# Performance work log

Hardware: AMD Instinct MI355X
Metric: run time of the kernel (lower is better)

## Reference

```python
import jax, jax.numpy as jnp
import numpy as np

N_NODES = 100000


def _gcn_norm(edge_index, n):
    # PyG GCNConv default: add self-loops, symmetric normalization
    src, dst = edge_index[0], edge_index[1]
    loops = jnp.arange(n, dtype=src.dtype)
    src = jnp.concatenate([src, loops])
    dst = jnp.concatenate([dst, loops])
    deg = jax.ops.segment_sum(jnp.ones_like(dst, dtype=jnp.float32), dst, num_segments=n)
    dinv = jnp.where(deg > 0, jax.lax.rsqrt(deg), 0.0)
    norm = dinv[src] * dinv[dst]  # [E+N]
    return src, dst, norm


def _gcn_conv(x, src, dst, norm, W, b, n):
    h = x @ W                                  # [N, out] transform first
    msg = h[src] * norm[:, None]               # gather + edge weight
    out = jax.ops.segment_sum(msg, dst, num_segments=n)  # scatter-add
    return out + b


def setup_inputs() -> dict:
    key = jax.random.key(0)
    k1, k2, k3, k4 = jax.random.split(key, 4)
    in_f, h_f, out_f = 128, 256, 128
    x = jax.random.normal(k1, (N_NODES, in_f), dtype=jnp.float32)
    edge_index = jax.random.randint(k2, (2, 1600000), 0, N_NODES, dtype=jnp.int64)
    W1 = jax.random.normal(k3, (in_f, h_f), dtype=jnp.float32) / np.sqrt(in_f)
    b1 = jnp.zeros((h_f,), dtype=jnp.float32)
    W2 = jax.random.normal(k4, (h_f, out_f), dtype=jnp.float32) / np.sqrt(h_f)
    b2 = jnp.zeros((out_f,), dtype=jnp.float32)
    return {"x": x, "edge_index": edge_index, "W1": W1, "b1": b1, "W2": W2, "b2": b2}


def reference(x, edge_index, W1, b1, W2, b2):
    n = x.shape[0]
    src, dst, norm = _gcn_norm(edge_index, n)
    h = jax.nn.relu(_gcn_conv(x, src, dst, norm, W1, b1, n))
    return _gcn_conv(h, src, dst, norm, W2, b2, n)
```

## Files before the change

kernel.cpp:

```cpp
#include <hip/hip_runtime.h>

typedef __bf16 bf16x8 __attribute__((ext_vector_type(8)));
typedef float f32x4 __attribute__((ext_vector_type(4)));

#define DEVI static __device__ __forceinline__
#define CHUNK 4096
#define SCH 8192

DEVI unsigned short f2bf(float f){
  unsigned int x = __builtin_bit_cast(unsigned int, f);
  x = (x + 0x7fffu + ((x >> 16) & 1u)) >> 16;
  return (unsigned short)x;
}
DEVI unsigned int packbf2(float a, float b){
  return (unsigned int)f2bf(a) | ((unsigned int)f2bf(b) << 16);
}
DEVI float bflo(unsigned int u){ return __builtin_bit_cast(float, u << 16); }
DEVI float bfhi(unsigned int u){ return __builtin_bit_cast(float, u & 0xffff0000u); }

__global__ void k_zero(int* __restrict__ p, int n){
  int i = blockIdx.x*256 + threadIdx.x;
  if (i < n) p[i] = 0;
}


__global__ __launch_bounds__(256) void kb_hist(const int* __restrict__ dst,
    int* __restrict__ bucketCnt, int E, int NB){
  __shared__ int h[2048];
  for (int i=threadIdx.x;i<NB;i+=256) h[i]=0;
  __syncthreads();
  int base = blockIdx.x*CHUNK;
  int lim = base+CHUNK < E ? base+CHUNK : E;
  for (int i = base+threadIdx.x; i < lim; i += 256)
    atomicAdd(&h[dst[i]>>8], 1);
  __syncthreads();
  for (int i=threadIdx.x;i<NB;i+=256)
    if (h[i]) atomicAdd(&bucketCnt[i], h[i]);
}

__global__ __launch_bounds__(256) void kb_scan(const int* __restrict__ bucketCnt,
    int* __restrict__ bucketOff, int* __restrict__ bucketCur,
    int* __restrict__ cCur, int NB, int NBC){
  __shared__ int sh[256];
  int t = threadIdx.x;
  int per = (NB+255)/256;
  int vals[8];
  int lsum = 0;
  for (int j=0;j<per;j++){
    int i = t*per+j;
    int v = (i<NB) ? bucketCnt[i] : 0;
    vals[j]=v; lsum+=v;
  }
  sh[t]=lsum; __syncthreads();
  for (int off=1; off<256; off<<=1){
    int x = (t>=off) ? sh[t-off] : 0;
    __syncthreads();
    sh[t] += x;
    __syncthreads();
  }
  int run = sh[t]-lsum;
  for (int j=0;j<per;j++){
    int i = t*per+j;
    if (i<NB){ bucketOff[i]=run; bucketCur[i]=run; }
    run += vals[j];
  }
  if (t==255) bucketOff[NB]=run;
  __syncthreads();
  for (int c=t;c<NBC;c+=256){
    int f = c*8;
    cCur[c] = bucketOff[f < NB ? f : NB];
  }
}

__global__ __launch_bounds__(512) void kb_scat1(const int* __restrict__ src,
    const int* __restrict__ dst, int* __restrict__ cur,
    int* __restrict__ p1, int E, int NBK){
  __shared__ int h[64];
  __shared__ int baseSh[64];
  int t = threadIdx.x;
  if (t < NBK){ h[t]=0; }
  __syncthreads();
  int base = blockIdx.x*SCH;
  int lim = base+SCH < E ? base+SCH : E;
  for (int i = base+t; i < lim; i += 512)
    atomicAdd(&h[dst[i]>>11], 1);
  __syncthreads();
  if (t < NBK){
    int c = h[t];
    baseSh[t] = c ? atomicAdd(&cur[t], c) : 0;
    h[t] = 0;
  }
  __syncthreads();
  for (int i = base+t; i < lim; i += 512){
    int d = dst[i];
    int b = d>>11;
    int r = atomicAdd(&h[b], 1);
    int p = baseSh[b] + r;
    p1[p] = (src[i]<<11) | (d & 2047);
  }
}

__global__ __launch_bounds__(512) void kb_scat2(const int* __restrict__ p1,
    const int* __restrict__ bOff, int* __restrict__ cur,
    int* __restrict__ pk, int NB){
  __shared__ int h[8];
  __shared__ int baseSh[8];
  int t = threadIdx.x;
  int bc = blockIdx.x >> 3;
  int sub = blockIdx.x & 7;
  int s = bOff[bc*8];
  int fe = bc*8+8; if (fe > NB) fe = NB;
  int e = bOff[fe];
  if (t < 8) h[t] = 0;
  __syncthreads();
  for (int i = s + sub*512 + t; i < e; i += 4096)
    atomicAdd(&h[(p1[i]>>8)&7], 1);
  __syncthreads();
  if (t < 8){
    int c2 = h[t];
    baseSh[t] = c2 ? atomicAdd(&cur[bc*8+t], c2) : 0;
    h[t] = 0;
  }
  __syncthreads();
  for (int i = s + sub*512 + t; i < e; i += 4096){
    int p = p1[i];
    int f = (p>>8)&7;
    int r = atomicAdd(&h[f], 1);
    int pos = baseSh[f] + r;
    pk[pos] = ((p>>11)<<8) | (p&255);
  }
}

DEVI void packW(const float* __restrict__ W, unsigned short* __restrict__ Wp,
                int idx, int N, int NF){
  int l = idx & 63;
  int frag = idx >> 6;
  int cf = frag % NF;
  int ks = frag / NF;
  int kbase = ks*32 + (l>>4)*8;
  int col = cf*16 + (l&15);
  unsigned short* dp = Wp + (size_t)idx*8;
  #pragma unroll
  for (int j=0;j<8;j++) dp[j] = f2bf(W[(size_t)(kbase+j)*N + col]);
}

__global__ __launch_bounds__(256) void kb_fused(const int* __restrict__ pk,
    const int* __restrict__ bOff,
    int* __restrict__ rp, int* __restrict__ csr, float* __restrict__ dinv,
    const float2* __restrict__ x2, unsigned int* __restrict__ xb,
    const float* __restrict__ W1, unsigned short* __restrict__ W1p,
    const float* __restrict__ W2, unsigned short* __restrict__ W2p,
    int n, int NB, int E){
  int t = threadIdx.x;
  int b = blockIdx.x;
  if (b >= NB){
    int idx = (b-NB)*256 + t;
    if (idx < 4096) packW(W1, W1p, idx, 256, 16);
    else            packW(W2, W2p, idx-4096, 128, 8);
    return;
  }
  __shared__ int c[256];
  __shared__ int sh[256];
  __shared__ int cur[256];
  __shared__ float dv[256];
  int s = bOff[b], e2 = bOff[b+1];
  c[t]=0; __syncthreads();
  for (int i=s+t;i<e2;i+=256) atomicAdd(&c[pk[i]&255], 1);
  __syncthreads();
  int deg = c[t];
  sh[t]=deg; __syncthreads();
  for (int o=1;o<256;o<<=1){
    int x = (t>=o) ? sh[t-o] : 0;
    __syncthreads();
    sh[t]+=x;
    __syncthreads();
  }
  int excl = sh[t]-deg;
  int node = b*256+t;
  float dnv = rsqrtf((float)(deg+1));
  if (node<n){
    rp[node] = s + excl;
    dinv[node] = dnv;
  }
  if (b==NB-1 && t==0) rp[n] = E;
  cur[t] = s + excl;
  dv[t] = dnv;
  __syncthreads();
  for (int i=s+t;i<e2;i+=256){
    int p = pk[i];
    int r = atomicAdd(&cur[p&255], 1);
    csr[r] = p & (int)0xFFFFFF00u;
  }
  int base_node = b*256;
  int rows = n - base_node; if (rows > 256) rows = 256;
  int j = t & 63;
  for (int rb = t>>6; rb < rows; rb += 4){
    int nd = base_node + rb;
    float d = dv[rb];
    float2 v = x2[(size_t)nd*64 + j];
    xb[(size_t)nd*64 + j] = packbf2(d*v.x, d*v.y);
  }
}

#define ACC8(V) { a0+=bflo(V.x); a1+=bfhi(V.x); a2+=bflo(V.y); a3+=bfhi(V.y); \
                  a4+=bflo(V.z); a5+=bfhi(V.z); a6+=bflo(V.w); a7+=bfhi(V.w); }

template<bool FINAL>
__global__ __launch_bounds__(256) void k_agg(
    const unsigned int* __restrict__ xs, const int* __restrict__ rp,
    const int* __restrict__ csr, const float* __restrict__ dinv,
    const float* __restrict__ bias, unsigned int* __restrict__ outb,
    float* __restrict__ outf, int n){
  int node = blockIdx.x*4 + (threadIdx.x>>6);
  if (node >= n) return;
  int l = threadIdx.x & 63;
  int q = l & 15;
  int h = l >> 4;
  const char* xbase = (const char*)xs;
  float a0=0,a1=0,a2=0,a3=0,a4=0,a5=0,a6=0,a7=0;
  int e = rp[node], end = rp[node+1];
  int p = e;
  int nf = (end - e) >> 4;
  for (int blk=0; blk<nf; ++blk, p+=16){
    uint4 v[4];
    #pragma unroll
    for (int i=0;i<4;i++){
      int boff = csr[p + 4*i + h];
      v[i] = *(const uint4*)(xbase + (size_t)(unsigned)boff + q*16);
    }
    ACC8(v[0]); ACC8(v[1]); ACC8(v[2]); ACC8(v[3]);
  }
  int rem = end - p;
  if (rem >= 8){
    uint4 v[2];
    #pragma unroll
    for (int i=0;i<2;i++){
      int boff = csr[p + 4*i + h];
      v[i] = *(const uint4*)(xbase + (size_t)(unsigned)boff + q*16);
    }
    ACC8(v[0]); ACC8(v[1]);
    p += 8; rem -= 8;
  }
  if (rem > 0){
    uint4 v[2];
    #pragma unroll
    for (int i=0;i<2;i++){
      int ei = p + 4*i + h;
      int ec = ei < end-1 ? ei : end-1;
      int boff = csr[ec];
      uint4 t = *(const uint4*)(xbase + (size_t)(unsigned)boff + q*16);
      if (ei >= end){ t.x=0; t.y=0; t.z=0; t.w=0; }
      v[i] = t;
    }
    ACC8(v[0]); ACC8(v[1]);
  }
  a0 += __shfl_xor(a0,16); a0 += __shfl_xor(a0,32);
  a1 += __shfl_xor(a1,16); a1 += __shfl_xor(a1,32);
  a2 += __shfl_xor(a2,16); a2 += __shfl_xor(a2,32);
  a3 += __shfl_xor(a3,16); a3 += __shfl_xor(a3,32);
  a4 += __shfl_xor(a4,16); a4 += __shfl_xor(a4,32);
  a5 += __shfl_xor(a5,16); a5 += __shfl_xor(a5,32);
  a6 += __shfl_xor(a6,16); a6 += __shfl_xor(a6,32);
  a7 += __shfl_xor(a7,16); a7 += __shfl_xor(a7,32);
  uint4 sv = *(const uint4*)(xbase + (size_t)node*256 + q*16);
  ACC8(sv);
  float dn = dinv[node];
  if constexpr (FINAL){
    if (h < 2){
      const float4 bb = *(const float4*)(bias + 8*q + 4*h);
      f32x4 r;
      r.x = (h ? a4 : a0)*dn + bb.x;
      r.y = (h ? a5 : a1)*dn + bb.y;
      r.z = (h ? a6 : a2)*dn + bb.z;
      r.w = (h ? a7 : a3)*dn + bb.w;
      __builtin_nontemporal_store(r, (f32x4*)(outf + (size_t)node*128 + 8*q + 4*h));
    }
  } else {
    if (h == 0){
      uint4 o;
      o.x = packbf2(a0*dn, a1*dn);
      o.y = packbf2(a2*dn, a3*dn);
      o.z = packbf2(a4*dn, a5*dn);
      o.w = packbf2(a6*dn, a7*dn);
      *(uint4*)((char*)outb + (size_t)node*256 + q*16) = o;
    }
  }
}

template<int K, int N, bool BIASRELU, bool ROWSCALE>
__global__ __launch_bounds__(256) void k_gemm(
    const unsigned short* __restrict__ A, const unsigned short* __restrict__ Wp,
    const float* __restrict__ bias, const float* __restrict__ rowscale,
    unsigned short* __restrict__ C, int M){
  constexpr int KS = K/32;
  constexpr int NF = N/16;
  constexpr int NWC = N/64;
  constexpr int NWR = 4/NWC;
  constexpr int BM = 64*NWR;
  int l = threadIdx.x & 63;
  int w = threadIdx.x >> 6;
  int wr = w / NWC, wc = w % NWC;
  int r0 = blockIdx.x*BM + wr*64;
  int c0 = wc*64;
  int lr = l & 15, lg = l >> 4;
  f32x4 acc[4][4];
  #pragma unroll
  for (int i=0;i<4;i++)
    #pragma unroll
    for (int j=0;j<4;j++)
      acc[i][j] = f32x4{0.f,0.f,0.f,0.f};
  for (int ks=0; ks<KS; ++ks){
    bf16x8 a[4], b[4];
    #pragma unroll
    for (int ar=0;ar<4;ar++){
      int row = r0 + ar*16 + lr;
      if (row > M-1) row = M-1;
      const uint4* p = (const uint4*)(A + (size_t)row*K + ks*32 + lg*8);
      union { uint4 u; bf16x8 v; } t; t.u = *p; a[ar] = t.v;
    }
    #pragma unroll
    for (int cb=0;cb<4;cb++){
      int cf = (c0>>4) + cb;
      const uint4* p = (const uint4*)(Wp + ((size_t)(ks*NF + cf)*64 + l)*8);
      union { uint4 u; bf16x8 v; } t; t.u = *p; b[cb] = t.v;
    }
    #pragma unroll
    for (int ar=0;ar<4;ar++)
      #pragma unroll
      for (int cb=0;cb<4;cb++)
        acc[ar][cb] = __builtin_amdgcn_mfma_f32_16x16x32_bf16(a[ar], b[cb], acc[ar][cb], 0, 0, 0);
  }
  #pragma unroll
  for (int ar=0;ar<4;ar++){
    #pragma unroll
    for (int i=0;i<4;i++){
      int row = r0 + ar*16 + lg*4 + i;
      if (row < M){
        float rs = 1.f;
        if constexpr (ROWSCALE) rs = rowscale[row];
        #pragma unroll
        for (int cb=0;cb<4;cb++){
          int col = c0 + cb*16 + lr;
          float v = acc[ar][cb][i];
          if constexpr (BIASRELU){ v += bias[col]; v = fmaxf(v, 0.f); }
          if constexpr (ROWSCALE) v *= rs;
          C[(size_t)row*N + col] = f2bf(v);
        }
      }
    }
  }
}

extern "C" void kernel_launch(void* const* d_in, const int* in_sizes, int n_in,
                              void* d_out, int out_size, void* d_ws, size_t ws_size,
                              hipStream_t stream){
  const float* x  = (const float*)d_in[0];
  const int*   ei = (const int*)d_in[1];
  const float* W1 = (const float*)d_in[2];
  const float* b1 = (const float*)d_in[3];
  const float* W2 = (const float*)d_in[4];
  const float* b2 = (const float*)d_in[5];
  const int IN_F = 128, H_F = 256, OUT_F = 128;
  int n = in_sizes[0] / IN_F;
  int E = in_sizes[1] / 2;
  const int* srcI = ei;
  const int* dstI = ei + E;
  const int NB  = (n+255)>>8;
  const int NBC = (n+2047)>>11;

  char* ws = (char*)d_ws;
  size_t off = 0;
  auto alloc = [&](size_t bytes)->char*{
    char* p = ws + off; off += (bytes + 255) & ~(size_t)255; return p;
  };
  int*   rp    = (int*)  alloc(((size_t)n+1)*4);
  float* dinv  = (float*)alloc((size_t)n*4);
  int*   bCnt  = (int*)  alloc((size_t)NB*4);
  int*   bOff  = (int*)  alloc(((size_t)NB+1)*4);
  int*   bCur  = (int*)  alloc((size_t)NB*4);
  int*   cCur  = (int*)  alloc(((size_t)NBC+1)*4);
  unsigned short* W1p = (unsigned short*)alloc((size_t)IN_F*H_F*2);
  unsigned short* W2p = (unsigned short*)alloc((size_t)H_F*OUT_F*2);
  int*   csr   = (int*)  alloc((size_t)E*4);
  unsigned int* xb = (unsigned int*)alloc((size_t)n*(IN_F/2)*4);
  unsigned int* AX = (unsigned int*)alloc((size_t)n*(IN_F/2)*4);
  unsigned short* H1 = (unsigned short*)alloc((size_t)n*H_F*2);
  int* p1 = (int*)H1;
  int* pk = p1 + E;

  int NCH = (E + CHUNK - 1)/CHUNK;
  int NSC = (E + SCH - 1)/SCH;

  k_zero<<<(NB+255)/256,256,0,stream>>>(bCnt, NB);
  kb_hist<<<NCH,256,0,stream>>>(dstI, bCnt, E, NB);
  kb_scan<<<1,256,0,stream>>>(bCnt, bOff, bCur, cCur, NB, NBC);
  kb_scat1<<<NSC,512,0,stream>>>(srcI, dstI, cCur, p1, E, NBC);
  kb_scat2<<<NBC*8,512,0,stream>>>(p1, bOff, bCur, pk, NB);
  kb_fused<<<NB+32,256,0,stream>>>(pk, bOff, rp, csr, dinv,
                                   (const float2*)x, xb, W1, W1p, W2, W2p, n, NB, E);
  k_agg<false><<<(n+3)/4,256,0,stream>>>(xb, rp, csr, dinv, nullptr, AX, nullptr, n);
  k_gemm<128,256,true,false><<<(n+63)/64,256,0,stream>>>((const unsigned short*)AX, W1p, b1, nullptr, H1, n);
  unsigned int* T = xb;
  k_gemm<256,128,false,true><<<(n+127)/128,256,0,stream>>>(H1, W2p, nullptr, dinv, (unsigned short*)T, n);
  k_agg<true><<<(n+3)/4,256,0,stream>>>(T, rp, csr, dinv, b2, nullptr, (float*)d_out, n);
}
```

Baseline: 261.2 us.

## Fuse two GEMMs via LDS and merge histogram into first scatter pass

```diff
diff --git a/kernel.cpp b/kernel.cpp
--- a/kernel.cpp
+++ b/kernel.cpp
@@ -4,8 +4,8 @@
 typedef float f32x4 __attribute__((ext_vector_type(4)));
 
 #define DEVI static __device__ __forceinline__
-#define CHUNK 4096
 #define SCH 8192
+#define CAP 49152
 
 DEVI unsigned short f2bf(float f){
   unsigned int x = __builtin_bit_cast(unsigned int, f);
@@ -24,23 +24,40 @@
 }
 
 
-__global__ __launch_bounds__(256) void kb_hist(const int* __restrict__ dst,
-    int* __restrict__ bucketCnt, int E, int NB){
-  __shared__ int h[2048];
-  for (int i=threadIdx.x;i<NB;i+=256) h[i]=0;
-  __syncthreads();
-  int base = blockIdx.x*CHUNK;
-  int lim = base+CHUNK < E ? base+CHUNK : E;
-  for (int i = base+threadIdx.x; i < lim; i += 256)
-    atomicAdd(&h[dst[i]>>8], 1);
-  __syncthreads();
-  for (int i=threadIdx.x;i<NB;i+=256)
-    if (h[i]) atomicAdd(&bucketCnt[i], h[i]);
-}
-
-__global__ __launch_bounds__(256) void kb_scan(const int* __restrict__ bucketCnt,
-    int* __restrict__ bucketOff, int* __restrict__ bucketCur,
-    int* __restrict__ cCur, int NB, int NBC){
+__global__ __launch_bounds__(512) void kb_scat1h(const int* __restrict__ src,
+    const int* __restrict__ dst, int* __restrict__ cntf, int* __restrict__ cntc,
+    int* __restrict__ p1, int E, int NB, int NBC){
+  __shared__ int hf[2048];
+  __shared__ int baseSh[64];
+  __shared__ int hc[64];
+  int t = threadIdx.x;
+  for (int i=t;i<NB;i+=512) hf[i]=0;
+  __syncthreads();
+  int base = blockIdx.x*SCH;
+  int lim = base+SCH < E ? base+SCH : E;
+  for (int i = base+t; i < lim; i += 512)
+    atomicAdd(&hf[dst[i]>>8], 1);
+  __syncthreads();
+  if (t < NBC){
+    int s2 = 0;
+    int f0 = t*8;
+    for (int j=0;j<8;j++){ int f=f0+j; if (f<NB) s2 += hf[f]; }
+    baseSh[t] = s2 ? atomicAdd(&cntc[t], s2) : 0;
+    hc[t] = 0;
+  }
+  for (int i=t;i<NB;i+=512)
+    if (hf[i]) atomicAdd(&cntf[i], hf[i]);
+  __syncthreads();
+  for (int i = base+t; i < lim; i += 512){
+    int d = dst[i];
+    int b = d>>11;
+    int r = atomicAdd(&hc[b], 1);
+    p1[(size_t)b*CAP + baseSh[b] + r] = (src[i]<<11) | (d & 2047);
+  }
+}
+
+__global__ __launch_bounds__(256) void kb_scan(const int* __restrict__ cntf,
+    int* __restrict__ bucketOff, int* __restrict__ bucketCur, int NB){
   __shared__ int sh[256];
   int t = threadIdx.x;
   int per = (NB+255)/256;
@@ -48,7 +65,7 @@
   int lsum = 0;
   for (int j=0;j<per;j++){
     int i = t*per+j;
-    int v = (i<NB) ? bucketCnt[i] : 0;
+    int v = (i<NB) ? cntf[i] : 0;
     vals[j]=v; lsum+=v;
   }
   sh[t]=lsum; __syncthreads();
@@ -65,52 +82,18 @@
     run += vals[j];
   }
   if (t==255) bucketOff[NB]=run;
-  __syncthreads();
-  for (int c=t;c<NBC;c+=256){
-    int f = c*8;
-    cCur[c] = bucketOff[f < NB ? f : NB];
-  }
-}
-
-__global__ __launch_bounds__(512) void kb_scat1(const int* __restrict__ src,
-    const int* __restrict__ dst, int* __restrict__ cur,
-    int* __restrict__ p1, int E, int NBK){
-  __shared__ int h[64];
-  __shared__ int baseSh[64];
-  int t = threadIdx.x;
-  if (t < NBK){ h[t]=0; }
-  __syncthreads();
-  int base = blockIdx.x*SCH;
-  int lim = base+SCH < E ? base+SCH : E;
-  for (int i = base+t; i < lim; i += 512)
-    atomicAdd(&h[dst[i]>>11], 1);
-  __syncthreads();
-  if (t < NBK){
-    int c = h[t];
-    baseSh[t] = c ? atomicAdd(&cur[t], c) : 0;
-    h[t] = 0;
-  }
-  __syncthreads();
-  for (int i = base+t; i < lim; i += 512){
-    int d = dst[i];
-    int b = d>>11;
-    int r = atomicAdd(&h[b], 1);
-    int p = baseSh[b] + r;
-    p1[p] = (src[i]<<11) | (d & 2047);
-  }
 }
 
 __global__ __launch_bounds__(512) void kb_scat2(const int* __restrict__ p1,
-    const int* __restrict__ bOff, int* __restrict__ cur,
+    const int* __restrict__ cntc, int* __restrict__ cur,
     int* __restrict__ pk, int NB){
   __shared__ int h[8];
   __shared__ int baseSh[8];
   int t = threadIdx.x;
   int bc = blockIdx.x >> 3;
   int sub = blockIdx.x & 7;
-  int s = bOff[bc*8];
-  int fe = bc*8+8; if (fe > NB) fe = NB;
-  int e = bOff[fe];
+  int s = bc*CAP;
+  int e = s + cntc[bc];
   if (t < 8) h[t] = 0;
   __syncthreads();
   for (int i = s + sub*512 + t; i < e; i += 4096)
@@ -287,64 +270,107 @@
   }
 }
 
-template<int K, int N, bool BIASRELU, bool ROWSCALE>
-__global__ __launch_bounds__(256) void k_gemm(
-    const unsigned short* __restrict__ A, const unsigned short* __restrict__ Wp,
-    const float* __restrict__ bias, const float* __restrict__ rowscale,
-    unsigned short* __restrict__ C, int M){
-  constexpr int KS = K/32;
-  constexpr int NF = N/16;
-  constexpr int NWC = N/64;
-  constexpr int NWR = 4/NWC;
-  constexpr int BM = 64*NWR;
+DEVI int ldsaddr(int row, int colg ){
+  int gs = (colg & ~7) | ((colg & 7) ^ (row & 7));
+  return row*512 + gs*16;
+}
+
+__global__ __launch_bounds__(256) void k_mlp(
+    const unsigned short* __restrict__ A, const unsigned short* __restrict__ W1p,
+    const float* __restrict__ b1, const unsigned short* __restrict__ W2p,
+    const float* __restrict__ dinv, unsigned short* __restrict__ T, int M){
+  __shared__ unsigned char At[64*512];
   int l = threadIdx.x & 63;
   int w = threadIdx.x >> 6;
-  int wr = w / NWC, wc = w % NWC;
-  int r0 = blockIdx.x*BM + wr*64;
-  int c0 = wc*64;
+  int r0 = blockIdx.x*64;
   int lr = l & 15, lg = l >> 4;
-  f32x4 acc[4][4];
-  #pragma unroll
-  for (int i=0;i<4;i++)
-    #pragma unroll
-    for (int j=0;j<4;j++)
-      acc[i][j] = f32x4{0.f,0.f,0.f,0.f};
-  for (int ks=0; ks<KS; ++ks){
-    bf16x8 a[4], b[4];
+  int c0 = w*64;
+  {
+    f32x4 acc[4][4];
+    #pragma unroll
+    for (int i=0;i<4;i++)
+      #pragma unroll
+      for (int j=0;j<4;j++)
+        acc[i][j] = f32x4{0.f,0.f,0.f,0.f};
+    #pragma unroll
+    for (int ks=0; ks<4; ++ks){
+      bf16x8 a[4], b[4];
+      #pragma unroll
+      for (int ar=0;ar<4;ar++){
+        int row = r0 + ar*16 + lr;
+        if (row > M-1) row = M-1;
+        const uint4* p = (const uint4*)(A + (size_t)row*128 + ks*32 + lg*8);
+        union { uint4 u; bf16x8 v; } t; t.u = *p; a[ar] = t.v;
+      }
+      #pragma unroll
+      for (int cb=0;cb<4;cb++){
+        int cf = (c0>>4) + cb;
+        const uint4* p = (const uint4*)(W1p + ((size_t)(ks*16 + cf)*64 + l)*8);
+        union { uint4 u; bf16x8 v; } t; t.u = *p; b[cb] = t.v;
+      }
+      #pragma unroll
+      for (int ar=0;ar<4;ar++)
+        #pragma unroll
+        for (int cb=0;cb<4;cb++)
+          acc[ar][cb] = __builtin_amdgcn_mfma_f32_16x16x32_bf16(a[ar], b[cb], acc[ar][cb], 0, 0, 0);
+    }
     #pragma unroll
     for (int ar=0;ar<4;ar++){
-      int row = r0 + ar*16 + lr;
-      if (row > M-1) row = M-1;
-      const uint4* p = (const uint4*)(A + (size_t)row*K + ks*32 + lg*8);
-      union { uint4 u; bf16x8 v; } t; t.u = *p; a[ar] = t.v;
-    }
-    #pragma unroll
-    for (int cb=0;cb<4;cb++){
-      int cf = (c0>>4) + cb;
-      const uint4* p = (const uint4*)(Wp + ((size_t)(ks*NF + cf)*64 + l)*8);
-      union { uint4 u; bf16x8 v; } t; t.u = *p; b[cb] = t.v;
-    }
-    #pragma unroll
-    for (int ar=0;ar<4;ar++)
-      #pragma unroll
-      for (int cb=0;cb<4;cb++)
-        acc[ar][cb] = __builtin_amdgcn_mfma_f32_16x16x32_bf16(a[ar], b[cb], acc[ar][cb], 0, 0, 0);
-  }
-  #pragma unroll
-  for (int ar=0;ar<4;ar++){
-    #pragma unroll
-    for (int i=0;i<4;i++){
-      int row = r0 + ar*16 + lg*4 + i;
-      if (row < M){
-        float rs = 1.f;
-        if constexpr (ROWSCALE) rs = rowscale[row];
+      #pragma unroll
+      for (int i=0;i<4;i++){
+        int row = ar*16 + lg*4 + i;
         #pragma unroll
         for (int cb=0;cb<4;cb++){
           int col = c0 + cb*16 + lr;
-          float v = acc[ar][cb][i];
-          if constexpr (BIASRELU){ v += bias[col]; v = fmaxf(v, 0.f); }
-          if constexpr (ROWSCALE) v *= rs;
-          C[(size_t)row*N + col] = f2bf(v);
+          float v = acc[ar][cb][i] + b1[col];
+          v = fmaxf(v, 0.f);
+          *(unsigned short*)(At + ldsaddr(row, col>>3) + (col&7)*2) = f2bf(v);
+        }
+      }
+    }
+  }
+  __syncthreads();
+  {
+    f32x4 acc[4][2];
+    #pragma unroll
+    for (int i=0;i<4;i++){
+      acc[i][0] = f32x4{0.f,0.f,0.f,0.f};
+      acc[i][1] = f32x4{0.f,0.f,0.f,0.f};
+    }
+    #pragma unroll
+    for (int ks=0; ks<8; ++ks){
+      bf16x8 a[4], b[2];
+      #pragma unroll
+      for (int ar=0;ar<4;ar++){
+        int row = ar*16 + lr;
+        union { uint4 u; bf16x8 v; } t;
+        t.u = *(const uint4*)(At + ldsaddr(row, ks*4 + lg));
+        a[ar] = t.v;
+      }
+      #pragma unroll
+      for (int cb=0;cb<2;cb++){
+        int cf = w*2 + cb;
+        const uint4* p = (const uint4*)(W2p + ((size_t)(ks*8 + cf)*64 + l)*8);
+        union { uint4 u; bf16x8 v; } t; t.u = *p; b[cb] = t.v;
+      }
+      #pragma unroll
+      for (int ar=0;ar<4;ar++){
+        acc[ar][0] = __builtin_amdgcn_mfma_f32_16x16x32_bf16(a[ar], b[0], acc[ar][0], 0, 0, 0);
+        acc[ar][1] = __builtin_amdgcn_mfma_f32_16x16x32_bf16(a[ar], b[1], acc[ar][1], 0, 0, 0);
+      }
+    }
+    #pragma unroll
+    for (int ar=0;ar<4;ar++){
+      #pragma unroll
+      for (int i=0;i<4;i++){
+        int row = r0 + ar*16 + lg*4 + i;
+        if (row < M){
+          float rs = dinv[row];
+          #pragma unroll
+          for (int cb=0;cb<2;cb++){
+            int col = w*32 + cb*16 + lr;
+            T[(size_t)row*128 + col] = f2bf(acc[ar][cb][i] * rs);
+          }
         }
       }
     }
@@ -360,7 +386,7 @@
   const float* b1 = (const float*)d_in[3];
   const float* W2 = (const float*)d_in[4];
   const float* b2 = (const float*)d_in[5];
-  const int IN_F = 128, H_F = 256, OUT_F = 128;
+  const int IN_F = 128;
   int n = in_sizes[0] / IN_F;
   int E = in_sizes[1] / 2;
   const int* srcI = ei;
@@ -375,32 +401,29 @@
   };
   int*   rp    = (int*)  alloc(((size_t)n+1)*4);
   float* dinv  = (float*)alloc((size_t)n*4);
-  int*   bCnt  = (int*)  alloc((size_t)NB*4);
+  int*   cntf  = (int*)  alloc(((size_t)NB+NBC)*4);
+  int*   cntc  = cntf + NB;
   int*   bOff  = (int*)  alloc(((size_t)NB+1)*4);
   int*   bCur  = (int*)  alloc((size_t)NB*4);
-  int*   cCur  = (int*)  alloc(((size_t)NBC+1)*4);
-  unsigned short* W1p = (unsigned short*)alloc((size_t)IN_F*H_F*2);
-  unsigned short* W2p = (unsigned short*)alloc((size_t)H_F*OUT_F*2);
+  unsigned short* W1p = (unsigned short*)alloc((size_t)128*256*2);
+  unsigned short* W2p = (unsigned short*)alloc((size_t)256*128*2);
   int*   csr   = (int*)  alloc((size_t)E*4);
-  unsigned int* xb = (unsigned int*)alloc((size_t)n*(IN_F/2)*4);
-  unsigned int* AX = (unsigned int*)alloc((size_t)n*(IN_F/2)*4);
-  unsigned short* H1 = (unsigned short*)alloc((size_t)n*H_F*2);
-  int* p1 = (int*)H1;
-  int* pk = p1 + E;
-
-  int NCH = (E + CHUNK - 1)/CHUNK;
+  unsigned int* xb = (unsigned int*)alloc((size_t)n*64*4);
+  unsigned int* AX = (unsigned int*)alloc((size_t)n*64*4);
+  int*   p1    = (int*)  alloc((size_t)NBC*CAP*4);
+  int*   pk    = (int*)  alloc((size_t)E*4);
+
   int NSC = (E + SCH - 1)/SCH;
 
-  k_zero<<<(NB+255)/256,256,0,stream>>>(bCnt, NB);
-  kb_hist<<<NCH,256,0,stream>>>(dstI, bCnt, E, NB);
-  kb_scan<<<1,256,0,stream>>>(bCnt, bOff, bCur, cCur, NB, NBC);
-  kb_scat1<<<NSC,512,0,stream>>>(srcI, dstI, cCur, p1, E, NBC);
-  kb_scat2<<<NBC*8,512,0,stream>>>(p1, bOff, bCur, pk, NB);
+  k_zero<<<(NB+NBC+255)/256,256,0,stream>>>(cntf, NB+NBC);
+  kb_scat1h<<<NSC,512,0,stream>>>(srcI, dstI, cntf, cntc, p1, E, NB, NBC);
+  kb_scan<<<1,256,0,stream>>>(cntf, bOff, bCur, NB);
+  kb_scat2<<<NBC*8,512,0,stream>>>(p1, cntc, bCur, pk, NB);
   kb_fused<<<NB+32,256,0,stream>>>(pk, bOff, rp, csr, dinv,
                                    (const float2*)x, xb, W1, W1p, W2, W2p, n, NB, E);
   k_agg<false><<<(n+3)/4,256,0,stream>>>(xb, rp, csr, dinv, nullptr, AX, nullptr, n);
-  k_gemm<128,256,true,false><<<(n+63)/64,256,0,stream>>>((const unsigned short*)AX, W1p, b1, nullptr, H1, n);
   unsigned int* T = xb;
-  k_gemm<256,128,false,true><<<(n+127)/128,256,0,stream>>>(H1, W2p, nullptr, dinv, (unsigned short*)T, n);
+  k_mlp<<<(n+63)/64,256,0,stream>>>((const unsigned short*)AX, W1p, b1, W2p,
+                                    dinv, (unsigned short*)T, n);
   k_agg<true><<<(n+3)/4,256,0,stream>>>(T, rp, csr, dinv, b2, nullptr, (float*)d_out, n);
 }
```

Measured after the change: 232.2 us, median of 2. 1.13x faster.
